# Kernel optimization log

Hardware: AMD Instinct MI355X
Metric: run time of the kernel (lower is better)

## Reference

```python
import jax, jax.numpy as jnp
import numpy as np

B_BATCH, N_ATOMS, N_CGS = 128, 512, 16


def setup_inputs() -> dict:
    key = jax.random.key(0)
    k0, k1, k2, k3, k4, k5 = jax.random.split(key, 6)
    npair = N_CGS * N_CGS
    soft_assign = jax.random.uniform(k0, (B_BATCH, N_ATOMS, N_CGS), dtype=jnp.float32)
    a = jax.random.uniform(k1, (B_BATCH, N_ATOMS, N_CGS), dtype=jnp.float32)
    assign_norm = a / a.sum(axis=-1, keepdims=True)  # row-normalized soft assignment
    xyz = jax.random.normal(k2, (B_BATCH, N_ATOMS, 3), dtype=jnp.float32)
    cg_xyz = jax.random.normal(k3, (B_BATCH, N_CGS, 3), dtype=jnp.float32)
    W = 0.01 * jax.random.normal(k4, (N_ATOMS, npair + npair * npair), dtype=jnp.float32)
    assign_idx = jax.random.randint(k5, (N_ATOMS,), 0, N_CGS)
    return {"soft_assign": soft_assign, "xyz": xyz, "cg_xyz": cg_xyz,
            "assign_norm": assign_norm, "W": W, "assign_idx": assign_idx}


def reference(soft_assign, xyz, cg_xyz, assign_norm, W, assign_idx):
    b, n_cgs = cg_xyz.shape[0], cg_xyz.shape[1]
    npair = n_cgs * n_cgs
    # pairwise displacement basis: basis[b,i,j] = cg_xyz[b,j] - cg_xyz[b,i]
    basis = cg_xyz[:, None, :, :] - cg_xyz[:, :, None, :]      # [b, nc, nc, 3]
    Bmat = basis.reshape(b, npair, 3)                          # [b, npair, 3]
    # cross basis: entry (p,q) = cross(Bmat[q], Bmat[p]) (matches torch Bij x Bjk)
    cross_basis = jnp.cross(Bmat[:, None, :, :], Bmat[:, :, None, :])  # [b,npair,npair,3]
    Bfull = jnp.concatenate([Bmat, cross_basis.reshape(b, npair * npair, 3)], axis=1)
    # dx_recon[b,n,e] = sum_j Bfull[b,j,e] * W[n,j]
    dx_recon = jnp.einsum('bje,nj->bne', Bfull, W)             # [b, n_atoms, 3]
    # per-CG mean offset weighted by soft assignment
    cg_offset = jnp.einsum('bin,bij->bjn', dx_recon, assign_norm)  # [b, n_cgs, 3]
    xyz_recon = cg_xyz[:, assign_idx, :] - cg_offset[:, assign_idx, :] + dx_recon
    return (soft_assign, xyz, xyz_recon)
```

## Files before the change

### kernel.cpp

```cpp
#include <hip/hip_runtime.h>

constexpr int NC = 16;
constexpr int NP = 256;
constexpr int PITCH = 264;
constexpr int NATOMS = 512;
constexpr int NB = 128;
constexpr int WROW = NP + NP * NP;
constexpr int ANP = 21;
constexpr int DXP = 5;

#define F4ADD(a, v) do { (a).x += (v).x; (a).y += (v).y; (a).z += (v).z; (a).w += (v).w; } while (0)
#define F4SUB(a, v) do { (a).x -= (v).x; (a).y -= (v).y; (a).z -= (v).z; (a).w -= (v).w; } while (0)

__global__ __launch_bounds__(256) void k_stream(const float* __restrict__ W,
                                                const float* __restrict__ soft_assign,
                                                const float* __restrict__ xyz,
                                                float* __restrict__ wcd,
                                                float* __restrict__ w1c,
                                                float* __restrict__ out_sa,
                                                float* __restrict__ out_xyz) {
    __shared__ float Hp[4][NC][PITCH];
    const int n = blockIdx.x;
    const int t = threadIdx.x;
    const int s = t >> 6;
    const int l = t & 63;

    ((float4*)out_sa)[n * 512 + t]       = ((const float4*)soft_assign)[n * 512 + t];
    ((float4*)out_sa)[n * 512 + 256 + t] = ((const float4*)soft_assign)[n * 512 + 256 + t];
    if (t < 96) {
        ((float4*)out_xyz)[n * 96 + t] = ((const float4*)xyz)[n * 96 + t];
    }
    if (t < NC) {
        const float* __restrict__ W1 = W + (size_t)n * WROW;
        float a1 = 0.f;
#pragma unroll
        for (int pi = 0; pi < NC; ++pi) a1 += W1[pi * NC + t];
#pragma unroll
        for (int pj = 0; pj < NC; ++pj) a1 -= W1[t * NC + pj];
        w1c[n * NC + t] = a1;
    }

    const float4* __restrict__ wp =
        (const float4*)W + ((size_t)n * 16448 + 64 + (size_t)(s * 64) * 64 + l);
    float4 h4[NC], hn4[4];
#pragma unroll
    for (int d = 0; d < NC; ++d) { h4[d].x = 0.f; h4[d].y = 0.f; h4[d].z = 0.f; h4[d].w = 0.f; }
#pragma unroll
    for (int g = 0; g < 4; ++g) { hn4[g].x = 0.f; hn4[g].y = 0.f; hn4[g].z = 0.f; hn4[g].w = 0.f; }
#pragma unroll
    for (int i = 0; i < 64; ++i) {
        const float4 v = wp[(size_t)i * 64];
        F4ADD(h4[i & 15], v);
        F4ADD(hn4[i >> 4], v);
    }
    switch (s) {
      case 0:
#pragma unroll
        for (int k = 0; k < 4; ++k) F4SUB(h4[k], hn4[k]);
        break;
      case 1:
#pragma unroll
        for (int k = 0; k < 4; ++k) F4SUB(h4[4 + k], hn4[k]);
        break;
      case 2:
#pragma unroll
        for (int k = 0; k < 4; ++k) F4SUB(h4[8 + k], hn4[k]);
        break;
      default:
#pragma unroll
        for (int k = 0; k < 4; ++k) F4SUB(h4[12 + k], hn4[k]);
        break;
    }
#pragma unroll
    for (int d = 0; d < NC; ++d) {
        *(float4*)(&Hp[s][d][4 * l]) = h4[d];
    }
    __syncthreads();

#pragma unroll
    for (int d = 0; d < NC; ++d) {
        Hp[0][d][t] += (Hp[1][d][t] + Hp[2][d][t]) + Hp[3][d][t];
    }
    __syncthreads();

    {
        const int d = t >> 4, c = t & 15;
        float rp = 0.f, rm = 0.f;
#pragma unroll
        for (int qi = 0; qi < NC; ++qi) rp += Hp[0][d][qi * NC + c];
#pragma unroll
        for (int qj = 0; qj < NC; ++qj) rm += Hp[0][d][c * NC + qj];
        wcd[n * NP + t] = rp - rm;
    }
}

__global__ __launch_bounds__(256) void k_dx(const float* __restrict__ cg_xyz,
                                            const float* __restrict__ wcd,
                                            const float* __restrict__ w1c,
                                            float* __restrict__ dxp) {
    __shared__ float xs[NC][4];
    __shared__ float cxs[64][4];
    const int b = blockIdx.x >> 2;
    const int q = blockIdx.x & 3;
    const int t = threadIdx.x;

    if (t < 48) xs[t / 3][t % 3] = cg_xyz[(size_t)b * NC * 3 + t];
    __syncthreads();
    if (t < 64) {
        const int m = q * 64 + t, c = m & 15, d = m >> 4;
        const float ax = xs[c][0], ay = xs[c][1], az = xs[c][2];
        const float bx = xs[d][0], by = xs[d][1], bz = xs[d][2];
        cxs[t][0] = ay * bz - az * by;
        cxs[t][1] = az * bx - ax * bz;
        cxs[t][2] = ax * by - ay * bx;
        cxs[t][3] = 0.f;
    }
    __syncthreads();

#pragma unroll
    for (int a = 0; a < 2; ++a) {
        const int n = a * 256 + t;
        const float4* __restrict__ w0 =
            (const float4*)(wcd + (size_t)n * NP + q * 64);
        float dx0 = 0.f, dx1 = 0.f, dx2 = 0.f;
#pragma unroll
        for (int k4 = 0; k4 < 16; ++k4) {
            const float4 w = w0[k4];
            const float4 c0 = *(const float4*)(&cxs[k4 * 4 + 0][0]);
            const float4 c1 = *(const float4*)(&cxs[k4 * 4 + 1][0]);
            const float4 c2 = *(const float4*)(&cxs[k4 * 4 + 2][0]);
            const float4 c3 = *(const float4*)(&cxs[k4 * 4 + 3][0]);
            dx0 += w.x * c0.x + w.y * c1.x + w.z * c2.x + w.w * c3.x;
            dx1 += w.x * c0.y + w.y * c1.y + w.z * c2.y + w.w * c3.y;
            dx2 += w.x * c0.z + w.y * c1.z + w.z * c2.z + w.w * c3.z;
        }
        if (q == 0) {
            const float* __restrict__ w1r = w1c + n * NC;
#pragma unroll
            for (int c = 0; c < NC; ++c) {
                const float wv = w1r[c];
                dx0 += wv * xs[c][0]; dx1 += wv * xs[c][1]; dx2 += wv * xs[c][2];
            }
        }
        float* __restrict__ op = dxp + (((size_t)q * NB + b) * NATOMS + n) * 3;
        op[0] = dx0; op[1] = dx1; op[2] = dx2;
    }
}

__global__ __launch_bounds__(512) void k_finish(const float* __restrict__ cg_xyz,
                                                const float* __restrict__ assign_norm,
                                                const int* __restrict__ assign_idx,
                                                const float* __restrict__ dxp,
                                                float* __restrict__ out_recon) {
    __shared__ float an_l[NATOMS][ANP];
    __shared__ float dxl[NATOMS][DXP];
    __shared__ float xs[NC][4];
    __shared__ float cgo_l[NC][4];
    const int b = blockIdx.x;
    const int t = threadIdx.x;

    {
        const float4* __restrict__ anr =
            (const float4*)(assign_norm + ((size_t)b * NATOMS + t) * NC);
#pragma unroll
        for (int i = 0; i < 4; ++i) {
            const float4 v = anr[i];
            an_l[t][4 * i + 0] = v.x; an_l[t][4 * i + 1] = v.y;
            an_l[t][4 * i + 2] = v.z; an_l[t][4 * i + 3] = v.w;
        }
    }
    if (t < 48) xs[t / 3][t % 3] = cg_xyz[(size_t)b * NC * 3 + t];

    float dx0, dx1, dx2;
    {
        const size_t s0 = (((size_t)0 * NB + b) * NATOMS + t) * 3;
        const size_t s1 = (((size_t)1 * NB + b) * NATOMS + t) * 3;
        const size_t s2 = (((size_t)2 * NB + b) * NATOMS + t) * 3;
        const size_t s3 = (((size_t)3 * NB + b) * NATOMS + t) * 3;
        dx0 = (dxp[s0 + 0] + dxp[s1 + 0]) + (dxp[s2 + 0] + dxp[s3 + 0]);
        dx1 = (dxp[s0 + 1] + dxp[s1 + 1]) + (dxp[s2 + 1] + dxp[s3 + 1]);
        dx2 = (dxp[s0 + 2] + dxp[s1 + 2]) + (dxp[s2 + 2] + dxp[s3 + 2]);
    }
    dxl[t][0] = dx0; dxl[t][1] = dx1; dxl[t][2] = dx2;
    __syncthreads();

    {
        const int j = t >> 5, g = t & 31;
        float p0 = 0.f, p1 = 0.f, p2 = 0.f;
#pragma unroll
        for (int k = 0; k < 16; ++k) {
            const int i = g + 32 * k;
            const float a = an_l[i][j];
            p0 += a * dxl[i][0];
            p1 += a * dxl[i][1];
            p2 += a * dxl[i][2];
        }
#pragma unroll
        for (int sh = 1; sh < 32; sh <<= 1) {
            p0 += __shfl_xor(p0, sh);
            p1 += __shfl_xor(p1, sh);
            p2 += __shfl_xor(p2, sh);
        }
        if (g == 0) { cgo_l[j][0] = p0; cgo_l[j][1] = p1; cgo_l[j][2] = p2; }
    }
    __syncthreads();

    const int ci = assign_idx[t];
    const float r0 = xs[ci][0] - cgo_l[ci][0] + dx0;
    const float r1 = xs[ci][1] - cgo_l[ci][1] + dx1;
    const float r2 = xs[ci][2] - cgo_l[ci][2] + dx2;
    const size_t ob = ((size_t)b * NATOMS + t) * 3;
    out_recon[ob + 0] = r0;
    out_recon[ob + 1] = r1;
    out_recon[ob + 2] = r2;
}

extern "C" void kernel_launch(void* const* d_in, const int* in_sizes, int n_in,
                              void* d_out, int out_size, void* d_ws, size_t ws_size,
                              hipStream_t stream) {
    (void)in_sizes; (void)n_in; (void)out_size; (void)ws_size;
    const float* soft_assign = (const float*)d_in[0];
    const float* xyz         = (const float*)d_in[1];
    const float* cg_xyz      = (const float*)d_in[2];
    const float* assign_norm = (const float*)d_in[3];
    const float* W           = (const float*)d_in[4];
    const int*   assign_idx  = (const int*)d_in[5];

    float* out       = (float*)d_out;
    float* out_sa    = out;
    float* out_xyz   = out + (size_t)NB * NATOMS * NC;
    float* out_recon = out_xyz + (size_t)NB * NATOMS * 3;

    float* wcd = (float*)d_ws;
    float* w1c = wcd + (size_t)NATOMS * NP;
    float* dxp = w1c + (size_t)NATOMS * NC;

    k_stream<<<dim3(NATOMS), dim3(256), 0, stream>>>(W, soft_assign, xyz,
                                                     wcd, w1c, out_sa, out_xyz);
    k_dx<<<dim3(NB * 4), dim3(256), 0, stream>>>(cg_xyz, wcd, w1c, dxp);
    k_finish<<<dim3(NB), dim3(512), 0, stream>>>(cg_xyz, assign_norm, assign_idx,
                                                 dxp, out_recon);
}
```

Baseline: 44.80 us.

## Fuse dx computation into finish kernel and move passthrough copies there

Merges the k_dx and k_finish kernels into one per-batch kernel in which each thread computes the full 256-term dx dot product for its atom directly from wcd. This removes the dxp partial-sum workspace round trip and one kernel launch. The soft_assign/xyz passthrough copies move out of the W-streaming kernel into the new kernel. The cost is that dx now runs on only 128 blocks with a longer serial loop per thread instead of 512 blocks, which reduces parallelism for that phase.

```diff
diff --git a/kernel.cpp b/kernel.cpp
--- a/kernel.cpp
+++ b/kernel.cpp
@@ -13,23 +13,14 @@
 #define F4SUB(a, v) do { (a).x -= (v).x; (a).y -= (v).y; (a).z -= (v).z; (a).w -= (v).w; } while (0)
 
 __global__ __launch_bounds__(256) void k_stream(const float* __restrict__ W,
-                                                const float* __restrict__ soft_assign,
-                                                const float* __restrict__ xyz,
                                                 float* __restrict__ wcd,
-                                                float* __restrict__ w1c,
-                                                float* __restrict__ out_sa,
-                                                float* __restrict__ out_xyz) {
+                                                float* __restrict__ w1c) {
     __shared__ float Hp[4][NC][PITCH];
     const int n = blockIdx.x;
     const int t = threadIdx.x;
     const int s = t >> 6;
     const int l = t & 63;
 
-    ((float4*)out_sa)[n * 512 + t]       = ((const float4*)soft_assign)[n * 512 + t];
-    ((float4*)out_sa)[n * 512 + 256 + t] = ((const float4*)soft_assign)[n * 512 + 256 + t];
-    if (t < 96) {
-        ((float4*)out_xyz)[n * 96 + t] = ((const float4*)xyz)[n * 96 + t];
-    }
     if (t < NC) {
         const float* __restrict__ W1 = W + (size_t)n * WROW;
         float a1 = 0.f;
@@ -94,20 +85,48 @@
     }
 }
 
-__global__ __launch_bounds__(256) void k_dx(const float* __restrict__ cg_xyz,
-                                            const float* __restrict__ wcd,
-                                            const float* __restrict__ w1c,
-                                            float* __restrict__ dxp) {
+__global__ __launch_bounds__(512) void k_recon2(const float* __restrict__ cg_xyz,
+                                                const float* __restrict__ assign_norm,
+                                                const int* __restrict__ assign_idx,
+                                                const float* __restrict__ wcd,
+                                                const float* __restrict__ w1c,
+                                                const float* __restrict__ soft_assign,
+                                                const float* __restrict__ xyz,
+                                                float* __restrict__ out_sa,
+                                                float* __restrict__ out_xyz,
+                                                float* __restrict__ out_recon) {
+    __shared__ float an_l[NATOMS][ANP];
+    __shared__ float dxl[NATOMS][DXP];
     __shared__ float xs[NC][4];
-    __shared__ float cxs[64][4];
-    const int b = blockIdx.x >> 2;
-    const int q = blockIdx.x & 3;
+    __shared__ float cxs[NP][4];
+    __shared__ float cgo_l[NC][4];
+    const int b = blockIdx.x;
     const int t = threadIdx.x;
 
+#pragma unroll
+    for (int k = 0; k < 4; ++k) {
+        ((float4*)out_sa)[b * 2048 + k * 512 + t] =
+            ((const float4*)soft_assign)[b * 2048 + k * 512 + t];
+    }
+    if (t < 384) {
+        ((float4*)out_xyz)[b * 384 + t] = ((const float4*)xyz)[b * 384 + t];
+    }
+
+    {
+        const float4* __restrict__ anr =
+            (const float4*)(assign_norm + ((size_t)b * NATOMS + t) * NC);
+#pragma unroll
+        for (int i = 0; i < 4; ++i) {
+            const float4 v = anr[i];
+            an_l[t][4 * i + 0] = v.x; an_l[t][4 * i + 1] = v.y;
+            an_l[t][4 * i + 2] = v.z; an_l[t][4 * i + 3] = v.w;
+        }
+    }
     if (t < 48) xs[t / 3][t % 3] = cg_xyz[(size_t)b * NC * 3 + t];
     __syncthreads();
-    if (t < 64) {
-        const int m = q * 64 + t, c = m & 15, d = m >> 4;
+
+    if (t < NP) {
+        const int c = t & 15, d = t >> 4;
         const float ax = xs[c][0], ay = xs[c][1], az = xs[c][2];
         const float bx = xs[d][0], by = xs[d][1], bz = xs[d][2];
         cxs[t][0] = ay * bz - az * by;
@@ -117,15 +136,12 @@
     }
     __syncthreads();
 
-#pragma unroll
-    for (int a = 0; a < 2; ++a) {
-        const int n = a * 256 + t;
-        const float4* __restrict__ w0 =
-            (const float4*)(wcd + (size_t)n * NP + q * 64);
-        float dx0 = 0.f, dx1 = 0.f, dx2 = 0.f;
-#pragma unroll
-        for (int k4 = 0; k4 < 16; ++k4) {
-            const float4 w = w0[k4];
+    float dx0 = 0.f, dx1 = 0.f, dx2 = 0.f;
+    {
+        const float4* __restrict__ wrow = (const float4*)(wcd + t * NP);
+#pragma unroll 8
+        for (int k4 = 0; k4 < 64; ++k4) {
+            const float4 w = wrow[k4];
             const float4 c0 = *(const float4*)(&cxs[k4 * 4 + 0][0]);
             const float4 c1 = *(const float4*)(&cxs[k4 * 4 + 1][0]);
             const float4 c2 = *(const float4*)(&cxs[k4 * 4 + 2][0]);
@@ -134,52 +150,12 @@
             dx1 += w.x * c0.y + w.y * c1.y + w.z * c2.y + w.w * c3.y;
             dx2 += w.x * c0.z + w.y * c1.z + w.z * c2.z + w.w * c3.z;
         }
-        if (q == 0) {
-            const float* __restrict__ w1r = w1c + n * NC;
-#pragma unroll
-            for (int c = 0; c < NC; ++c) {
-                const float wv = w1r[c];
-                dx0 += wv * xs[c][0]; dx1 += wv * xs[c][1]; dx2 += wv * xs[c][2];
-            }
-        }
-        float* __restrict__ op = dxp + (((size_t)q * NB + b) * NATOMS + n) * 3;
-        op[0] = dx0; op[1] = dx1; op[2] = dx2;
-    }
-}
-
-__global__ __launch_bounds__(512) void k_finish(const float* __restrict__ cg_xyz,
-                                                const float* __restrict__ assign_norm,
-                                                const int* __restrict__ assign_idx,
-                                                const float* __restrict__ dxp,
-                                                float* __restrict__ out_recon) {
-    __shared__ float an_l[NATOMS][ANP];
-    __shared__ float dxl[NATOMS][DXP];
-    __shared__ float xs[NC][4];
-    __shared__ float cgo_l[NC][4];
-    const int b = blockIdx.x;
-    const int t = threadIdx.x;
-
-    {
-        const float4* __restrict__ anr =
-            (const float4*)(assign_norm + ((size_t)b * NATOMS + t) * NC);
-#pragma unroll
-        for (int i = 0; i < 4; ++i) {
-            const float4 v = anr[i];
-            an_l[t][4 * i + 0] = v.x; an_l[t][4 * i + 1] = v.y;
-            an_l[t][4 * i + 2] = v.z; an_l[t][4 * i + 3] = v.w;
-        }
-    }
-    if (t < 48) xs[t / 3][t % 3] = cg_xyz[(size_t)b * NC * 3 + t];
-
-    float dx0, dx1, dx2;
-    {
-        const size_t s0 = (((size_t)0 * NB + b) * NATOMS + t) * 3;
-        const size_t s1 = (((size_t)1 * NB + b) * NATOMS + t) * 3;
-        const size_t s2 = (((size_t)2 * NB + b) * NATOMS + t) * 3;
-        const size_t s3 = (((size_t)3 * NB + b) * NATOMS + t) * 3;
-        dx0 = (dxp[s0 + 0] + dxp[s1 + 0]) + (dxp[s2 + 0] + dxp[s3 + 0]);
-        dx1 = (dxp[s0 + 1] + dxp[s1 + 1]) + (dxp[s2 + 1] + dxp[s3 + 1]);
-        dx2 = (dxp[s0 + 2] + dxp[s1 + 2]) + (dxp[s2 + 2] + dxp[s3 + 2]);
+        const float* __restrict__ w1row = w1c + t * NC;
+#pragma unroll
+        for (int c = 0; c < NC; ++c) {
+            const float wv = w1row[c];
+            dx0 += wv * xs[c][0]; dx1 += wv * xs[c][1]; dx2 += wv * xs[c][2];
+        }
     }
     dxl[t][0] = dx0; dxl[t][1] = dx1; dxl[t][2] = dx2;
     __syncthreads();
@@ -233,11 +209,9 @@
 
     float* wcd = (float*)d_ws;
     float* w1c = wcd + (size_t)NATOMS * NP;
-    float* dxp = w1c + (size_t)NATOMS * NC;
-
-    k_stream<<<dim3(NATOMS), dim3(256), 0, stream>>>(W, soft_assign, xyz,
-                                                     wcd, w1c, out_sa, out_xyz);
-    k_dx<<<dim3(NB * 4), dim3(256), 0, stream>>>(cg_xyz, wcd, w1c, dxp);
-    k_finish<<<dim3(NB), dim3(512), 0, stream>>>(cg_xyz, assign_norm, assign_idx,
-                                                 dxp, out_recon);
+
+    k_stream<<<dim3(NATOMS), dim3(256), 0, stream>>>(W, wcd, w1c);
+    k_recon2<<<dim3(NB), dim3(512), 0, stream>>>(cg_xyz, assign_norm, assign_idx,
+                                                 wcd, w1c, soft_assign, xyz,
+                                                 out_sa, out_xyz, out_recon);
 }
```

After: 50.58 us. 1.13x slower.
